# Performance work log

Hardware: AMD Instinct MI355X
Metric: run time of the kernel (lower is better)

The kernel has to match this reference:

```python
import jax, jax.numpy as jnp
import numpy as np

M, N, D_MODEL = 16, 2048, 512
H, D = 8, 64  # num_heads, head_dim; inner_dim = H*D = 512


def setup_inputs() -> dict:
    key = jax.random.key(0)
    ks = jax.random.split(key, 8)
    s = 1.0 / np.sqrt(D_MODEL)
    return {
        "xq": jax.random.normal(ks[0], (M, N, D_MODEL), jnp.float32),
        "xk": jax.random.normal(ks[1], (M, N, D_MODEL), jnp.float32),
        "xv": jax.random.normal(ks[2], (M, N, D_MODEL), jnp.float32),
        "Wq": jax.random.normal(ks[3], (D_MODEL, H * D), jnp.float32) * s,
        "Wk": jax.random.normal(ks[4], (D_MODEL, H * D), jnp.float32) * s,
        "Wv": jax.random.normal(ks[5], (D_MODEL, H * D), jnp.float32) * s,
        "Wo": jax.random.normal(ks[6], (H * D, D_MODEL), jnp.float32) * s,
        "bo": jnp.zeros((D_MODEL,), jnp.float32),
    }


def _split_heads(x):
    # [m, n, h*d] -> [m, h, n, d]
    m, n, _ = x.shape
    return x.reshape(m, n, H, D).transpose(0, 2, 1, 3)


def reference(xq, xk, xv, Wq, Wk, Wv, Wo, bo):
    scale = D ** -0.5
    q = _split_heads(xq @ Wq)
    k = _split_heads(xk @ Wk)
    v = _split_heads(xv @ Wv)
    # linear attention: softmax over feature dim for both q and k
    q = jax.nn.softmax(q, axis=-1) * scale
    k = jax.nn.softmax(k, axis=-1)
    kv = jnp.einsum('mhnd,mhne->mhde', k, v)   # [m, h, d, d]
    out = jnp.einsum('mhqd,mhde->mhqe', q, kv)  # [m, h, nq, d]
    out = out.transpose(0, 2, 1, 3).reshape(out.shape[0], -1, H * D)
    return out @ Wo + bo
```

## Files before the change

### kernel.cpp

```cpp
#include <hip/hip_runtime.h>
#include <hip/hip_bf16.h>


typedef __bf16 bf16;
typedef __bf16 bf16x8 __attribute__((ext_vector_type(8)));
typedef __bf16 bf16x4 __attribute__((ext_vector_type(4)));
typedef float  f32x4  __attribute__((ext_vector_type(4)));

#define MFMA16(a, b, c) __builtin_amdgcn_mfma_f32_16x16x32_bf16((a), (b), (c), 0, 0, 0)

__device__ inline void glds16(const void* g, void* l) {
  __builtin_amdgcn_global_load_lds((const __attribute__((address_space(1))) void*)g,
                                   (__attribute__((address_space(3))) void*)l, 16, 0, 0);
}

__global__ __launch_bounds__(256) void k_prep(const float* __restrict__ w0, const float* __restrict__ w1,
                                              const float* __restrict__ w2, const float* __restrict__ w3,
                                              bf16* __restrict__ t0, bf16* __restrict__ t1,
                                              bf16* __restrict__ t2, bf16* __restrict__ t3)
{
  const float* W = (blockIdx.z == 0) ? w0 : (blockIdx.z == 1) ? w1 : (blockIdx.z == 2) ? w2 : w3;
  bf16*        T = (blockIdx.z == 0) ? t0 : (blockIdx.z == 1) ? t1 : (blockIdx.z == 2) ? t2 : t3;
  __shared__ float lds[64][68];
  const int t = threadIdx.x;
  const int r = t >> 2, c0 = (t & 3) << 4;
  const float* src = W + (size_t)(blockIdx.x * 64 + r) * 512 + blockIdx.y * 64 + c0;
  float4 f0 = ((const float4*)src)[0];
  float4 f1 = ((const float4*)src)[1];
  float4 f2 = ((const float4*)src)[2];
  float4 f3 = ((const float4*)src)[3];
  *(float4*)&lds[r][c0 + 0]  = f0;
  *(float4*)&lds[r][c0 + 4]  = f1;
  *(float4*)&lds[r][c0 + 8]  = f2;
  *(float4*)&lds[r][c0 + 12] = f3;
  __syncthreads();
  bf16 v[16];
#pragma unroll
  for (int s = 0; s < 16; ++s) v[s] = (bf16)lds[c0 + s][r];
  bf16* dst = T + (size_t)(blockIdx.y * 64 + r) * 512 + blockIdx.x * 64 + c0;
  *(bf16x8*)&dst[0] = *(bf16x8*)&v[0];
  *(bf16x8*)&dst[8] = *(bf16x8*)&v[8];
}

__global__ __launch_bounds__(512) void k_qkv(const float* __restrict__ xq, const float* __restrict__ xk,
                                             const float* __restrict__ xv,
                                             const bf16* __restrict__ WqT, const bf16* __restrict__ WkT,
                                             const bf16* __restrict__ WvT,
                                             bf16* __restrict__ Qo, bf16* __restrict__ Ko,
                                             bf16* __restrict__ Vo)
{
  const int proj = blockIdx.z;
  const float* X  = (proj == 0) ? xq  : (proj == 1) ? xk  : xv;
  const bf16*  WT = (proj == 0) ? WqT : (proj == 1) ? WkT : WvT;
  bf16*       OUT = (proj == 0) ? Qo  : (proj == 1) ? Ko  : Vo;

  __shared__ bf16 As[64][40];
  __shared__ bf16 Bs[512 * 32];

  const int t = threadIdx.x;
  const int lane = t & 63, w = t >> 6;
  const int g = lane >> 4, li = lane & 15;
  const size_t arow = (size_t)blockIdx.x * 64;

  const int ar = t >> 3, ac = (t & 7) << 2;
  const float* xp = X + (arow + ar) * 512 + ac;

  const bf16* bsrc = WT + (size_t)(w * 64 + (lane >> 2)) * 512
                        + (((lane & 3) ^ ((lane >> 3) & 3)) << 3);
  char* bdst = (char*)&Bs[0] + w * 4096;
  const int bslot = g ^ ((li >> 1) & 3);

  f32x4 acc[4][4] = {};
  float4 xa = ((const float4*)xp)[0];

  for (int kt = 0; kt < 16; ++kt) {
    __syncthreads();
    {
      bf16x4 h; h[0] = (bf16)xa.x; h[1] = (bf16)xa.y; h[2] = (bf16)xa.z; h[3] = (bf16)xa.w;
      *(bf16x4*)&As[ar][ac] = h;
    }
#pragma unroll
    for (int j = 0; j < 4; ++j)
      glds16(bsrc + (size_t)j * 16 * 512 + kt * 32, bdst + j * 1024);
    __syncthreads();
    if (kt < 15)
      xa = ((const float4*)(xp + (kt + 1) * 32))[0];
    bf16x8 af[4], bfr[4];
#pragma unroll
    for (int rt = 0; rt < 4; ++rt) af[rt] = *(const bf16x8*)&As[rt * 16 + li][g * 8];
#pragma unroll
    for (int ct = 0; ct < 4; ++ct)
      bfr[ct] = *(const bf16x8*)&Bs[(w * 64 + ct * 16 + li) * 32 + bslot * 8];
#pragma unroll
    for (int rt = 0; rt < 4; ++rt)
#pragma unroll
      for (int ct = 0; ct < 4; ++ct)
        acc[rt][ct] = MFMA16(af[rt], bfr[ct], acc[rt][ct]);
  }

#pragma unroll
  for (int rt = 0; rt < 4; ++rt) {
#pragma unroll
    for (int q = 0; q < 4; ++q) {
      float v0 = acc[rt][0][q], v1 = acc[rt][1][q], v2 = acc[rt][2][q], v3 = acc[rt][3][q];
      if (proj < 2) {
        float mx = fmaxf(fmaxf(v0, v1), fmaxf(v2, v3));
        mx = fmaxf(mx, __shfl_xor(mx, 1));
        mx = fmaxf(mx, __shfl_xor(mx, 2));
        mx = fmaxf(mx, __shfl_xor(mx, 4));
        mx = fmaxf(mx, __shfl_xor(mx, 8));
        v0 = __expf(v0 - mx); v1 = __expf(v1 - mx); v2 = __expf(v2 - mx); v3 = __expf(v3 - mx);
        float s = v0 + v1 + v2 + v3;
        s += __shfl_xor(s, 1); s += __shfl_xor(s, 2); s += __shfl_xor(s, 4); s += __shfl_xor(s, 8);
        const float inv = (proj == 0 ? 0.125f : 1.0f) / s;
        v0 *= inv; v1 *= inv; v2 *= inv; v3 *= inv;
      }
      bf16* o = OUT + (arow + rt * 16 + g * 4 + q) * 512 + w * 64 + li;
      o[0] = (bf16)v0; o[16] = (bf16)v1; o[32] = (bf16)v2; o[48] = (bf16)v3;
    }
  }
}

__global__ __launch_bounds__(256) void k_kv(const bf16* __restrict__ K, const bf16* __restrict__ V,
                                            float* __restrict__ kvp)
{
  const int mh = blockIdx.x, m = mh >> 3, h = mh & 7;
  const int ns = blockIdx.y;
  __shared__ bf16 Kt[64][40];
  __shared__ bf16 Vt[64][40];
  const int t = threadIdx.x, lane = t & 63, wave = t >> 6;
  const int dq = wave >> 1, eq = wave & 1;
  const int g = lane >> 4, li = lane & 15;
  const int tn = t & 31, d0 = (t >> 5) << 3;
  const size_t rowbase = (size_t)m * 2048 + ns * 512;

  f32x4 acc[2][2] = {};

  for (int nt = 0; nt < 16; ++nt) {
    __syncthreads();
    {
      bf16x8 kr = *(const bf16x8*)(K + (rowbase + nt * 32 + tn) * 512 + h * 64 + d0);
      bf16x8 vr = *(const bf16x8*)(V + (rowbase + nt * 32 + tn) * 512 + h * 64 + d0);
#pragma unroll
      for (int j = 0; j < 8; ++j) Kt[d0 + j][tn] = kr[j];
#pragma unroll
      for (int j = 0; j < 8; ++j) Vt[d0 + j][tn] = vr[j];
    }
    __syncthreads();
    bf16x8 af[2], bfr[2];
#pragma unroll
    for (int dt = 0; dt < 2; ++dt) af[dt]  = *(const bf16x8*)&Kt[dq * 32 + dt * 16 + li][g * 8];
#pragma unroll
    for (int et = 0; et < 2; ++et) bfr[et] = *(const bf16x8*)&Vt[eq * 32 + et * 16 + li][g * 8];
#pragma unroll
    for (int dt = 0; dt < 2; ++dt)
#pragma unroll
      for (int et = 0; et < 2; ++et)
        acc[dt][et] = MFMA16(af[dt], bfr[et], acc[dt][et]);
  }

  float* o = kvp + ((size_t)mh * 4 + ns) * 4096;
#pragma unroll
  for (int dt = 0; dt < 2; ++dt)
#pragma unroll
    for (int et = 0; et < 2; ++et)
#pragma unroll
      for (int q = 0; q < 4; ++q) {
        const int d = dq * 32 + dt * 16 + g * 4 + q;
        const int e = eq * 32 + et * 16 + li;
        o[d * 64 + e] = acc[dt][et][q];
      }
}

__global__ __launch_bounds__(512) void k_wfused(const float* __restrict__ kvp, const bf16* __restrict__ WoT,
                                                bf16* __restrict__ WfT)
{
  const int mh = blockIdx.x, m = mh >> 3, h = mh & 7;
  __shared__ bf16 kvs[64][72];
  const int t = threadIdx.x, lane = t & 63, wave = t >> 6;
  const int g = lane >> 4, li = lane & 15;
  {
    const int d = t >> 3, e0 = (t & 7) << 3;
    const float* p = kvp + (size_t)mh * 16384 + d * 64 + e0;
#pragma unroll
    for (int j = 0; j < 8; ++j) {
      float s = p[j] + p[4096 + j] + p[8192 + j] + p[12288 + j];
      kvs[d][e0 + j] = (bf16)s;
    }
  }
  __syncthreads();
  f32x4 acc[4][4] = {};
#pragma unroll
  for (int kk = 0; kk < 2; ++kk) {
    bf16x8 af[4], bfr[4];
#pragma unroll
    for (int rt = 0; rt < 4; ++rt) {
      const int c = wave * 64 + rt * 16 + li;
      af[rt] = *(const bf16x8*)(WoT + (size_t)c * 512 + h * 64 + kk * 32 + g * 8);
    }
#pragma unroll
    for (int ct = 0; ct < 4; ++ct)
      bfr[ct] = *(const bf16x8*)&kvs[ct * 16 + li][kk * 32 + g * 8];
#pragma unroll
    for (int rt = 0; rt < 4; ++rt)
#pragma unroll
      for (int ct = 0; ct < 4; ++ct)
        acc[rt][ct] = MFMA16(af[rt], bfr[ct], acc[rt][ct]);
  }
  bf16* o = WfT + (size_t)m * 262144;
#pragma unroll
  for (int rt = 0; rt < 4; ++rt)
#pragma unroll
    for (int ct = 0; ct < 4; ++ct)
#pragma unroll
      for (int q = 0; q < 4; ++q) {
        const int c = wave * 64 + rt * 16 + g * 4 + q;
        const int r = h * 64 + ct * 16 + li;
        o[(size_t)c * 512 + r] = (bf16)acc[rt][ct][q];
      }
}

__global__ __launch_bounds__(512) void k_out(const bf16* __restrict__ Q, const bf16* __restrict__ WfT,
                                             const float* __restrict__ bo, float* __restrict__ out)
{
  const int rb = blockIdx.x;
  const int m  = rb >> 5;
  const bf16* Bm = WfT + (size_t)m * 262144;

  __shared__ bf16 As[64 * 64];
  __shared__ bf16 Bs[512 * 64];

  const int t = threadIdx.x, lane = t & 63, w = t >> 6;
  const int g = lane >> 4, li = lane & 15;
  const size_t arow = (size_t)rb * 64;

  const int lr = lane >> 3, ls = lane & 7;
  const int schunk = ls ^ lr;
  const bf16* asrc = Q  + (arow + w * 8 + lr) * 512 + schunk * 8;
  const bf16* bsrc = Bm + (size_t)(w * 64 + lr) * 512 + schunk * 8;
  char* adst = (char*)&As[0] + w * 1024;
  char* bdst = (char*)&Bs[0] + w * 8192;

  f32x4 acc[4][4] = {};

  for (int kt = 0; kt < 8; ++kt) {
    __syncthreads();
    glds16(asrc + kt * 64, adst);
#pragma unroll
    for (int j = 0; j < 8; ++j)
      glds16(bsrc + (size_t)j * 8 * 512 + kt * 64, bdst + j * 1024);
    __syncthreads();
#pragma unroll
    for (int ks = 0; ks < 2; ++ks) {
      bf16x8 af[4], bfr[4];
#pragma unroll
      for (int rt = 0; rt < 4; ++rt) {
        const int r = rt * 16 + li;
        af[rt] = *(const bf16x8*)&As[r * 64 + ((ks * 4 + g) ^ (li & 7)) * 8];
      }
#pragma unroll
      for (int ct = 0; ct < 4; ++ct) {
        const int c = w * 64 + ct * 16 + li;
        bfr[ct] = *(const bf16x8*)&Bs[c * 64 + ((ks * 4 + g) ^ (li & 7)) * 8];
      }
#pragma unroll
      for (int rt = 0; rt < 4; ++rt)
#pragma unroll
        for (int ct = 0; ct < 4; ++ct)
          acc[rt][ct] = MFMA16(af[rt], bfr[ct], acc[rt][ct]);
    }
  }

  float bv[4];
#pragma unroll
  for (int ct = 0; ct < 4; ++ct) bv[ct] = bo[w * 64 + ct * 16 + li];
#pragma unroll
  for (int rt = 0; rt < 4; ++rt)
#pragma unroll
    for (int q = 0; q < 4; ++q) {
      float* o = out + (arow + rt * 16 + g * 4 + q) * 512 + w * 64 + li;
      o[0]  = acc[rt][0][q] + bv[0];
      o[16] = acc[rt][1][q] + bv[1];
      o[32] = acc[rt][2][q] + bv[2];
      o[48] = acc[rt][3][q] + bv[3];
    }
}

extern "C" void kernel_launch(void* const* d_in, const int* in_sizes, int n_in,
                              void* d_out, int out_size, void* d_ws, size_t ws_size,
                              hipStream_t stream)
{
  const float* xq = (const float*)d_in[0];
  const float* xk = (const float*)d_in[1];
  const float* xv = (const float*)d_in[2];
  const float* Wq = (const float*)d_in[3];
  const float* Wk = (const float*)d_in[4];
  const float* Wv = (const float*)d_in[5];
  const float* Wo = (const float*)d_in[6];
  const float* bo = (const float*)d_in[7];
  float* out = (float*)d_out;

  char* ws = (char*)d_ws;
  const size_t WT_BYTES  = 512 * 512 * 2;
  const size_t QKV_BYTES = (size_t)32768 * 512 * 2;
  bf16*  WqT = (bf16*)(ws);
  bf16*  WkT = (bf16*)(ws + WT_BYTES);
  bf16*  WvT = (bf16*)(ws + 2 * WT_BYTES);
  bf16*  WoT = (bf16*)(ws + 3 * WT_BYTES);
  bf16*  Qb  = (bf16*)(ws + 4 * WT_BYTES);
  bf16*  Kb  = (bf16*)(ws + 4 * WT_BYTES + QKV_BYTES);
  bf16*  Vb  = (bf16*)(ws + 4 * WT_BYTES + 2 * QKV_BYTES);
  float* kvp = (float*)(ws + 4 * WT_BYTES + 3 * QKV_BYTES);
  bf16*  WfT = Kb;

  k_prep  <<<dim3(8, 8, 4),   256, 0, stream>>>(Wq, Wk, Wv, Wo, WqT, WkT, WvT, WoT);
  k_qkv   <<<dim3(512, 1, 3), 512, 0, stream>>>(xq, xk, xv, WqT, WkT, WvT, Qb, Kb, Vb);
  k_kv    <<<dim3(128, 4),    256, 0, stream>>>(Kb, Vb, kvp);
  k_wfused<<<dim3(128),       512, 0, stream>>>(kvp, WoT, WfT);
  k_out   <<<dim3(512),       512, 0, stream>>>(Qb, WfT, bo, out);
}
```

Baseline: 166.9 us.

## Double-buffer LDS tiles with async global-to-LDS loads in QKV and output GEMMs

Both the QKV projection GEMM and the output GEMM now keep two LDS buffers and prefetch the next K-slice with global_load_lds while MFMAs run on the current one, so each step needs one wait/barrier instead of two __syncthreads. In k_qkv the fp32 activations are copied straight into swizzled LDS and converted to bf16 at fragment-load time, replacing the register round-trip. k_out moves from 64-wide to 32-wide K steps to fit the double buffers. Both kernels declare launch_bounds(512,2), which caps registers, and the larger LDS footprint could limit occupancy.

```diff
diff --git a/kernel.cpp b/kernel.cpp
--- a/kernel.cpp
+++ b/kernel.cpp
@@ -8,6 +8,13 @@
 typedef float  f32x4  __attribute__((ext_vector_type(4)));
 
 #define MFMA16(a, b, c) __builtin_amdgcn_mfma_f32_16x16x32_bf16((a), (b), (c), 0, 0, 0)
+
+__device__ inline bf16x8 cvt8(float4 a, float4 b) {
+  bf16x8 h;
+  h[0] = (bf16)a.x; h[1] = (bf16)a.y; h[2] = (bf16)a.z; h[3] = (bf16)a.w;
+  h[4] = (bf16)b.x; h[5] = (bf16)b.y; h[6] = (bf16)b.z; h[7] = (bf16)b.w;
+  return h;
+}
 
 __device__ inline void glds16(const void* g, void* l) {
   __builtin_amdgcn_global_load_lds((const __attribute__((address_space(1))) void*)g,
@@ -42,60 +49,71 @@
   *(bf16x8*)&dst[8] = *(bf16x8*)&v[8];
 }
 
-__global__ __launch_bounds__(512) void k_qkv(const float* __restrict__ xq, const float* __restrict__ xk,
-                                             const float* __restrict__ xv,
-                                             const bf16* __restrict__ WqT, const bf16* __restrict__ WkT,
-                                             const bf16* __restrict__ WvT,
-                                             bf16* __restrict__ Qo, bf16* __restrict__ Ko,
-                                             bf16* __restrict__ Vo)
+__global__ __launch_bounds__(512, 2) void k_qkv(const float* __restrict__ xq, const float* __restrict__ xk,
+                                                const float* __restrict__ xv,
+                                                const bf16* __restrict__ WqT, const bf16* __restrict__ WkT,
+                                                const bf16* __restrict__ WvT,
+                                                bf16* __restrict__ Qo, bf16* __restrict__ Ko,
+                                                bf16* __restrict__ Vo)
 {
   const int proj = blockIdx.z;
   const float* X  = (proj == 0) ? xq  : (proj == 1) ? xk  : xv;
   const bf16*  WT = (proj == 0) ? WqT : (proj == 1) ? WkT : WvT;
   bf16*       OUT = (proj == 0) ? Qo  : (proj == 1) ? Ko  : Vo;
 
-  __shared__ bf16 As[64][40];
-  __shared__ bf16 Bs[512 * 32];
+  __shared__ float Af[2][2048];
+  __shared__ bf16  Bsm[2][16384];
 
   const int t = threadIdx.x;
   const int lane = t & 63, w = t >> 6;
   const int g = lane >> 4, li = lane & 15;
   const size_t arow = (size_t)blockIdx.x * 64;
 
-  const int ar = t >> 3, ac = (t & 7) << 2;
-  const float* xp = X + (arow + ar) * 512 + ac;
-
+  const float* asrc = X + (size_t)(arow + w * 8 + (lane >> 3)) * 512
+                        + (((lane & 7) ^ ((lane >> 3) & 7)) << 2);
   const bf16* bsrc = WT + (size_t)(w * 64 + (lane >> 2)) * 512
                         + (((lane & 3) ^ ((lane >> 3) & 3)) << 3);
-  char* bdst = (char*)&Bs[0] + w * 4096;
-  const int bslot = g ^ ((li >> 1) & 3);
 
   f32x4 acc[4][4] = {};
-  float4 xa = ((const float4*)xp)[0];
-
+
+#pragma unroll
+  for (int j = 0; j < 4; ++j)
+    glds16(bsrc + (size_t)j * 16 * 512, (char*)&Bsm[0][0] + w * 4096 + j * 1024);
+  glds16(asrc, (char*)&Af[0][0] + w * 1024);
+  asm volatile("s_waitcnt vmcnt(0)" ::: "memory");
+  __builtin_amdgcn_s_barrier();
+
+#pragma unroll
   for (int kt = 0; kt < 16; ++kt) {
-    __syncthreads();
-    {
-      bf16x4 h; h[0] = (bf16)xa.x; h[1] = (bf16)xa.y; h[2] = (bf16)xa.z; h[3] = (bf16)xa.w;
-      *(bf16x4*)&As[ar][ac] = h;
-    }
-#pragma unroll
-    for (int j = 0; j < 4; ++j)
-      glds16(bsrc + (size_t)j * 16 * 512 + kt * 32, bdst + j * 1024);
-    __syncthreads();
-    if (kt < 15)
-      xa = ((const float4*)(xp + (kt + 1) * 32))[0];
+    const int cur = kt & 1;
+    if (kt < 15) {
+#pragma unroll
+      for (int j = 0; j < 4; ++j)
+        glds16(bsrc + (size_t)j * 16 * 512 + (kt + 1) * 32,
+               (char*)&Bsm[cur ^ 1][0] + w * 4096 + j * 1024);
+      glds16(asrc + (kt + 1) * 32, (char*)&Af[cur ^ 1][0] + w * 1024);
+    }
     bf16x8 af[4], bfr[4];
-#pragma unroll
-    for (int rt = 0; rt < 4; ++rt) af[rt] = *(const bf16x8*)&As[rt * 16 + li][g * 8];
+    const float* Ab = &Af[cur][0];
+#pragma unroll
+    for (int rt = 0; rt < 4; ++rt) {
+      const int r = rt * 16 + li;
+      float4 a0 = *(const float4*)&Ab[r * 32 + (((2 * g)    ) ^ (li & 7)) * 4];
+      float4 a1 = *(const float4*)&Ab[r * 32 + (((2 * g) | 1) ^ (li & 7)) * 4];
+      af[rt] = cvt8(a0, a1);
+    }
 #pragma unroll
     for (int ct = 0; ct < 4; ++ct)
-      bfr[ct] = *(const bf16x8*)&Bs[(w * 64 + ct * 16 + li) * 32 + bslot * 8];
+      bfr[ct] = *(const bf16x8*)&Bsm[cur][(w * 64 + ct * 16 + li) * 32 + (g ^ ((li >> 1) & 3)) * 8];
 #pragma unroll
     for (int rt = 0; rt < 4; ++rt)
 #pragma unroll
       for (int ct = 0; ct < 4; ++ct)
         acc[rt][ct] = MFMA16(af[rt], bfr[ct], acc[rt][ct]);
+    if (kt < 15) {
+      asm volatile("s_waitcnt vmcnt(0)" ::: "memory");
+      __builtin_amdgcn_s_barrier();
+    }
   }
 
 #pragma unroll
@@ -220,54 +238,59 @@
       }
 }
 
-__global__ __launch_bounds__(512) void k_out(const bf16* __restrict__ Q, const bf16* __restrict__ WfT,
-                                             const float* __restrict__ bo, float* __restrict__ out)
+__global__ __launch_bounds__(512, 2) void k_out(const bf16* __restrict__ Q, const bf16* __restrict__ WfT,
+                                                const float* __restrict__ bo, float* __restrict__ out)
 {
   const int rb = blockIdx.x;
   const int m  = rb >> 5;
   const bf16* Bm = WfT + (size_t)m * 262144;
 
-  __shared__ bf16 As[64 * 64];
-  __shared__ bf16 Bs[512 * 64];
+  __shared__ bf16 Ab2[2][2048];
+  __shared__ bf16 Bb2[2][16384];
 
   const int t = threadIdx.x, lane = t & 63, w = t >> 6;
   const int g = lane >> 4, li = lane & 15;
   const size_t arow = (size_t)rb * 64;
 
-  const int lr = lane >> 3, ls = lane & 7;
-  const int schunk = ls ^ lr;
-  const bf16* asrc = Q  + (arow + w * 8 + lr) * 512 + schunk * 8;
-  const bf16* bsrc = Bm + (size_t)(w * 64 + lr) * 512 + schunk * 8;
-  char* adst = (char*)&As[0] + w * 1024;
-  char* bdst = (char*)&Bs[0] + w * 8192;
+  const bf16* asrc = Q + (arow + w * 16 + (lane >> 2)) * 512
+                       + (((lane & 3) ^ ((lane >> 2) & 3)) << 3);
+  const bf16* bsrc = Bm + (size_t)(w * 64 + (lane >> 2)) * 512
+                        + (((lane & 3) ^ ((lane >> 3) & 3)) << 3);
 
   f32x4 acc[4][4] = {};
 
-  for (int kt = 0; kt < 8; ++kt) {
-    __syncthreads();
-    glds16(asrc + kt * 64, adst);
-#pragma unroll
-    for (int j = 0; j < 8; ++j)
-      glds16(bsrc + (size_t)j * 8 * 512 + kt * 64, bdst + j * 1024);
-    __syncthreads();
-#pragma unroll
-    for (int ks = 0; ks < 2; ++ks) {
-      bf16x8 af[4], bfr[4];
-#pragma unroll
-      for (int rt = 0; rt < 4; ++rt) {
-        const int r = rt * 16 + li;
-        af[rt] = *(const bf16x8*)&As[r * 64 + ((ks * 4 + g) ^ (li & 7)) * 8];
-      }
-#pragma unroll
-      for (int ct = 0; ct < 4; ++ct) {
-        const int c = w * 64 + ct * 16 + li;
-        bfr[ct] = *(const bf16x8*)&Bs[c * 64 + ((ks * 4 + g) ^ (li & 7)) * 8];
-      }
-#pragma unroll
-      for (int rt = 0; rt < 4; ++rt)
-#pragma unroll
-        for (int ct = 0; ct < 4; ++ct)
-          acc[rt][ct] = MFMA16(af[rt], bfr[ct], acc[rt][ct]);
+#pragma unroll
+  for (int j = 0; j < 4; ++j)
+    glds16(bsrc + (size_t)j * 16 * 512, (char*)&Bb2[0][0] + w * 4096 + j * 1024);
+  if (w < 4) glds16(asrc, (char*)&Ab2[0][0] + w * 1024);
+  asm volatile("s_waitcnt vmcnt(0)" ::: "memory");
+  __builtin_amdgcn_s_barrier();
+
+#pragma unroll
+  for (int kt = 0; kt < 16; ++kt) {
+    const int cur = kt & 1;
+    if (kt < 15) {
+#pragma unroll
+      for (int j = 0; j < 4; ++j)
+        glds16(bsrc + (size_t)j * 16 * 512 + (kt + 1) * 32,
+               (char*)&Bb2[cur ^ 1][0] + w * 4096 + j * 1024);
+      if (w < 4) glds16(asrc + (kt + 1) * 32, (char*)&Ab2[cur ^ 1][0] + w * 1024);
+    }
+    bf16x8 af[4], bfr[4];
+#pragma unroll
+    for (int rt = 0; rt < 4; ++rt)
+      af[rt] = *(const bf16x8*)&Ab2[cur][(rt * 16 + li) * 32 + (g ^ (li & 3)) * 8];
+#pragma unroll
+    for (int ct = 0; ct < 4; ++ct)
+      bfr[ct] = *(const bf16x8*)&Bb2[cur][(w * 64 + ct * 16 + li) * 32 + (g ^ ((li >> 1) & 3)) * 8];
+#pragma unroll
+    for (int rt = 0; rt < 4; ++rt)
+#pragma unroll
+      for (int ct = 0; ct < 4; ++ct)
+        acc[rt][ct] = MFMA16(af[rt], bfr[ct], acc[rt][ct]);
+    if (kt < 15) {
+      asm volatile("s_waitcnt vmcnt(0)" ::: "memory");
+      __builtin_amdgcn_s_barrier();
     }
   }
 
```

Measured after the change: 221.1 us. 1.33x slower.

## Retile QKV and output GEMMs to 128x256 blocks with XCD-aware block remapping

Applied to the files above, without the earlier changes.

Changes the QKV projection and output GEMM tiles from 64x512 to 128x256 per workgroup, arranged as a 2x4 wave grid. Each block now loads half as much weight data per K step while reading more activation rows, which rebalances A/B operand reuse. Block indices are remapped so that consecutive blocks on the same XCD work on nearby rows, aiming for better L2 locality. The output kernel also moves from 64-wide to 32-wide K steps, which doubles the number of barrier-synchronised iterations.

```diff
diff --git a/kernel.cpp b/kernel.cpp
--- a/kernel.cpp
+++ b/kernel.cpp
@@ -8,6 +8,13 @@
 typedef float  f32x4  __attribute__((ext_vector_type(4)));
 
 #define MFMA16(a, b, c) __builtin_amdgcn_mfma_f32_16x16x32_bf16((a), (b), (c), 0, 0, 0)
+
+__device__ inline bf16x8 cvt8(float4 a, float4 b) {
+  bf16x8 h;
+  h[0] = (bf16)a.x; h[1] = (bf16)a.y; h[2] = (bf16)a.z; h[3] = (bf16)a.w;
+  h[4] = (bf16)b.x; h[5] = (bf16)b.y; h[6] = (bf16)b.z; h[7] = (bf16)b.w;
+  return h;
+}
 
 __device__ inline void glds16(const void* g, void* l) {
   __builtin_amdgcn_global_load_lds((const __attribute__((address_space(1))) void*)g,
@@ -49,48 +56,55 @@
                                              bf16* __restrict__ Qo, bf16* __restrict__ Ko,
                                              bf16* __restrict__ Vo)
 {
-  const int proj = blockIdx.z;
+  const int wg = blockIdx.x;
+  const int o  = (wg & 7) * 192 + (wg >> 3);
+  const int proj = o >> 9;
+  const int rem  = o & 511;
+  const int rb = rem >> 1, cb = rem & 1;
+
   const float* X  = (proj == 0) ? xq  : (proj == 1) ? xk  : xv;
   const bf16*  WT = (proj == 0) ? WqT : (proj == 1) ? WkT : WvT;
   bf16*       OUT = (proj == 0) ? Qo  : (proj == 1) ? Ko  : Vo;
 
-  __shared__ bf16 As[64][40];
-  __shared__ bf16 Bs[512 * 32];
+  __shared__ bf16 As[128][40];
+  __shared__ bf16 Bs[256 * 32];
 
   const int t = threadIdx.x;
   const int lane = t & 63, w = t >> 6;
+  const int wr = w >> 2, wc = w & 3;
   const int g = lane >> 4, li = lane & 15;
-  const size_t arow = (size_t)blockIdx.x * 64;
-
-  const int ar = t >> 3, ac = (t & 7) << 2;
+  const size_t arow = (size_t)rb * 128;
+
+  const int ar = t >> 2, ac = (t & 3) << 3;
   const float* xp = X + (arow + ar) * 512 + ac;
 
-  const bf16* bsrc = WT + (size_t)(w * 64 + (lane >> 2)) * 512
+  const bf16* bsrc = WT + (size_t)(cb * 256 + w * 32 + (lane >> 2)) * 512
                         + (((lane & 3) ^ ((lane >> 3) & 3)) << 3);
-  char* bdst = (char*)&Bs[0] + w * 4096;
+  char* bdst = (char*)&Bs[0] + w * 2048;
   const int bslot = g ^ ((li >> 1) & 3);
 
   f32x4 acc[4][4] = {};
-  float4 xa = ((const float4*)xp)[0];
+  float4 xa0 = ((const float4*)xp)[0];
+  float4 xa1 = ((const float4*)xp)[1];
 
   for (int kt = 0; kt < 16; ++kt) {
     __syncthreads();
-    {
-      bf16x4 h; h[0] = (bf16)xa.x; h[1] = (bf16)xa.y; h[2] = (bf16)xa.z; h[3] = (bf16)xa.w;
-      *(bf16x4*)&As[ar][ac] = h;
-    }
-#pragma unroll
-    for (int j = 0; j < 4; ++j)
+    *(bf16x8*)&As[ar][ac] = cvt8(xa0, xa1);
+#pragma unroll
+    for (int j = 0; j < 2; ++j)
       glds16(bsrc + (size_t)j * 16 * 512 + kt * 32, bdst + j * 1024);
     __syncthreads();
-    if (kt < 15)
-      xa = ((const float4*)(xp + (kt + 1) * 32))[0];
+    if (kt < 15) {
+      xa0 = ((const float4*)(xp + (kt + 1) * 32))[0];
+      xa1 = ((const float4*)(xp + (kt + 1) * 32))[1];
+    }
     bf16x8 af[4], bfr[4];
 #pragma unroll
-    for (int rt = 0; rt < 4; ++rt) af[rt] = *(const bf16x8*)&As[rt * 16 + li][g * 8];
+    for (int rt = 0; rt < 4; ++rt)
+      af[rt] = *(const bf16x8*)&As[wr * 64 + rt * 16 + li][g * 8];
 #pragma unroll
     for (int ct = 0; ct < 4; ++ct)
-      bfr[ct] = *(const bf16x8*)&Bs[(w * 64 + ct * 16 + li) * 32 + bslot * 8];
+      bfr[ct] = *(const bf16x8*)&Bs[(wc * 64 + ct * 16 + li) * 32 + bslot * 8];
 #pragma unroll
     for (int rt = 0; rt < 4; ++rt)
 #pragma unroll
@@ -115,8 +129,8 @@
         const float inv = (proj == 0 ? 0.125f : 1.0f) / s;
         v0 *= inv; v1 *= inv; v2 *= inv; v3 *= inv;
       }
-      bf16* o = OUT + (arow + rt * 16 + g * 4 + q) * 512 + w * 64 + li;
-      o[0] = (bf16)v0; o[16] = (bf16)v1; o[32] = (bf16)v2; o[48] = (bf16)v3;
+      bf16* op = OUT + (arow + wr * 64 + rt * 16 + g * 4 + q) * 512 + cb * 256 + wc * 64 + li;
+      op[0] = (bf16)v0; op[16] = (bf16)v1; op[32] = (bf16)v2; op[48] = (bf16)v3;
     }
   }
 }
@@ -223,66 +237,62 @@
 __global__ __launch_bounds__(512) void k_out(const bf16* __restrict__ Q, const bf16* __restrict__ WfT,
                                              const float* __restrict__ bo, float* __restrict__ out)
 {
-  const int rb = blockIdx.x;
-  const int m  = rb >> 5;
+  const int wg = blockIdx.x;
+  const int o  = (wg & 7) * 64 + (wg >> 3);
+  const int rb = o >> 1, cb = o & 1;
+  const int m  = rb >> 4;
   const bf16* Bm = WfT + (size_t)m * 262144;
 
-  __shared__ bf16 As[64 * 64];
-  __shared__ bf16 Bs[512 * 64];
+  __shared__ bf16 As2[128 * 32];
+  __shared__ bf16 Bs2[256 * 32];
 
   const int t = threadIdx.x, lane = t & 63, w = t >> 6;
+  const int wr = w >> 2, wc = w & 3;
   const int g = lane >> 4, li = lane & 15;
-  const size_t arow = (size_t)rb * 64;
-
-  const int lr = lane >> 3, ls = lane & 7;
-  const int schunk = ls ^ lr;
-  const bf16* asrc = Q  + (arow + w * 8 + lr) * 512 + schunk * 8;
-  const bf16* bsrc = Bm + (size_t)(w * 64 + lr) * 512 + schunk * 8;
-  char* adst = (char*)&As[0] + w * 1024;
-  char* bdst = (char*)&Bs[0] + w * 8192;
+  const size_t arow = (size_t)rb * 128;
+
+  const int schunk = ((lane & 3) ^ ((lane >> 3) & 3)) << 3;
+  const bf16* asrc = Q + (arow + w * 16 + (lane >> 2)) * 512 + schunk;
+  const bf16* bsrc = Bm + (size_t)(cb * 256 + w * 32 + (lane >> 2)) * 512 + schunk;
+  char* adst = (char*)&As2[0] + w * 1024;
+  char* bdst = (char*)&Bs2[0] + w * 2048;
+  const int slot = g ^ ((li >> 1) & 3);
 
   f32x4 acc[4][4] = {};
 
-  for (int kt = 0; kt < 8; ++kt) {
-    __syncthreads();
-    glds16(asrc + kt * 64, adst);
-#pragma unroll
-    for (int j = 0; j < 8; ++j)
-      glds16(bsrc + (size_t)j * 8 * 512 + kt * 64, bdst + j * 1024);
-    __syncthreads();
-#pragma unroll
-    for (int ks = 0; ks < 2; ++ks) {
-      bf16x8 af[4], bfr[4];
-#pragma unroll
-      for (int rt = 0; rt < 4; ++rt) {
-        const int r = rt * 16 + li;
-        af[rt] = *(const bf16x8*)&As[r * 64 + ((ks * 4 + g) ^ (li & 7)) * 8];
-      }
-#pragma unroll
-      for (int ct = 0; ct < 4; ++ct) {
-        const int c = w * 64 + ct * 16 + li;
-        bfr[ct] = *(const bf16x8*)&Bs[c * 64 + ((ks * 4 + g) ^ (li & 7)) * 8];
-      }
-#pragma unroll
-      for (int rt = 0; rt < 4; ++rt)
-#pragma unroll
-        for (int ct = 0; ct < 4; ++ct)
-          acc[rt][ct] = MFMA16(af[rt], bfr[ct], acc[rt][ct]);
-    }
+  for (int kt = 0; kt < 16; ++kt) {
+    __syncthreads();
+    glds16(asrc + kt * 32, adst);
+#pragma unroll
+    for (int j = 0; j < 2; ++j)
+      glds16(bsrc + (size_t)j * 16 * 512 + kt * 32, bdst + j * 1024);
+    __syncthreads();
+    bf16x8 af[4], bfr[4];
+#pragma unroll
+    for (int rt = 0; rt < 4; ++rt)
+      af[rt] = *(const bf16x8*)&As2[(wr * 64 + rt * 16 + li) * 32 + slot * 8];
+#pragma unroll
+    for (int ct = 0; ct < 4; ++ct)
+      bfr[ct] = *(const bf16x8*)&Bs2[(wc * 64 + ct * 16 + li) * 32 + slot * 8];
+#pragma unroll
+    for (int rt = 0; rt < 4; ++rt)
+#pragma unroll
+      for (int ct = 0; ct < 4; ++ct)
+        acc[rt][ct] = MFMA16(af[rt], bfr[ct], acc[rt][ct]);
   }
 
   float bv[4];
 #pragma unroll
-  for (int ct = 0; ct < 4; ++ct) bv[ct] = bo[w * 64 + ct * 16 + li];
+  for (int ct = 0; ct < 4; ++ct) bv[ct] = bo[cb * 256 + wc * 64 + ct * 16 + li];
 #pragma unroll
   for (int rt = 0; rt < 4; ++rt)
 #pragma unroll
     for (int q = 0; q < 4; ++q) {
-      float* o = out + (arow + rt * 16 + g * 4 + q) * 512 + w * 64 + li;
-      o[0]  = acc[rt][0][q] + bv[0];
-      o[16] = acc[rt][1][q] + bv[1];
-      o[32] = acc[rt][2][q] + bv[2];
-      o[48] = acc[rt][3][q] + bv[3];
+      float* op = out + (arow + wr * 64 + rt * 16 + g * 4 + q) * 512 + cb * 256 + wc * 64 + li;
+      op[0]  = acc[rt][0][q] + bv[0];
+      op[16] = acc[rt][1][q] + bv[1];
+      op[32] = acc[rt][2][q] + bv[2];
+      op[48] = acc[rt][3][q] + bv[3];
     }
 }
 
@@ -313,9 +323,9 @@
   float* kvp = (float*)(ws + 4 * WT_BYTES + 3 * QKV_BYTES);
   bf16*  WfT = Kb;
 
-  k_prep  <<<dim3(8, 8, 4),   256, 0, stream>>>(Wq, Wk, Wv, Wo, WqT, WkT, WvT, WoT);
-  k_qkv   <<<dim3(512, 1, 3), 512, 0, stream>>>(xq, xk, xv, WqT, WkT, WvT, Qb, Kb, Vb);
-  k_kv    <<<dim3(128, 4),    256, 0, stream>>>(Kb, Vb, kvp);
-  k_wfused<<<dim3(128),       512, 0, stream>>>(kvp, WoT, WfT);
-  k_out   <<<dim3(512),       512, 0, stream>>>(Qb, WfT, bo, out);
-}
+  k_prep  <<<dim3(8, 8, 4), 256, 0, stream>>>(Wq, Wk, Wv, Wo, WqT, WkT, WvT, WoT);
+  k_qkv   <<<dim3(1536),    512, 0, stream>>>(xq, xk, xv, WqT, WkT, WvT, Qb, Kb, Vb);
+  k_kv    <<<dim3(128, 4),  256, 0, stream>>>(Kb, Vb, kvp);
+  k_wfused<<<dim3(128),     512, 0, stream>>>(kvp, WoT, WfT);
+  k_out   <<<dim3(512),     512, 0, stream>>>(Qb, WfT, bo, out);
+}
```

After: 164.5 us (median of 2 runs). Within noise of the previous version (-1.4%).
